# Optimization experiments

Hardware: AMD Instinct MI355X
Metric: run time of the kernel (lower is better)

## Reference

```python
import jax, jax.numpy as jnp
import numpy as np

B_, N, C, H = 8192, 49, 192, 6
HD = C // H
SCALE = HD ** -0.5


def setup_inputs() -> dict:
    key = jax.random.key(0)
    k0, k1, k2, k3 = jax.random.split(key, 4)
    x = jax.random.normal(k0, (B_, N, C), dtype=jnp.float32)
    mask = jax.random.randint(k1, (B_, N), 0, 2, dtype=jnp.int32)
    w_qkv = jax.random.normal(k2, (C, 3 * C), dtype=jnp.float32) * 0.02
    b_qkv = jnp.zeros((3 * C,), dtype=jnp.float32)
    w_proj = jax.random.normal(k3, (C, C), dtype=jnp.float32) * 0.02
    b_proj = jnp.zeros((C,), dtype=jnp.float32)
    return {"x": x, "mask": mask, "w_qkv": w_qkv, "b_qkv": b_qkv,
            "w_proj": w_proj, "b_proj": b_proj}


def reference(x, mask, w_qkv, b_qkv, w_proj, b_proj):
    # qkv projection: [B_, N, 3C] -> [3, B_, H, N, HD]
    qkv = (x @ w_qkv + b_qkv).reshape(B_, N, 3, H, HD).transpose(2, 0, 3, 1, 4)
    q, k, v = qkv[0], qkv[1], qkv[2]
    # scaled QK^T: [B_, H, N, N]
    attn = jnp.einsum('bhnd,bhmd->bhnm', q, k) * SCALE
    # additive key mask: mask==0 positions get -inf
    attn = jnp.where(mask[:, None, None, :] == 0, -jnp.inf, attn)
    p = jax.nn.softmax(attn, axis=-1)  # dropout p=0 -> identity
    out = jnp.einsum('bhnm,bhmd->bhnd', p, v)  # AV
    out = out.transpose(0, 2, 1, 3).reshape(B_, N, C)
    return out @ w_proj + b_proj
```

## Files before the change

kernel.cpp:

```cpp
#include <hip/hip_runtime.h>


typedef __attribute__((ext_vector_type(8))) short short8;
typedef __attribute__((ext_vector_type(4))) float f32x4;

#define SCALE 0.17677669529663687f

__device__ __forceinline__ unsigned short f2bf(float x) {
    union { float f; unsigned int i; } v; v.f = x;
    return (unsigned short)((v.i + 0x7FFFu + ((v.i >> 16) & 1u)) >> 16);
}

__device__ __forceinline__ unsigned int pkbf(float lo, float hi) {
    unsigned int r;
    asm("v_cvt_pk_bf16_f32 %0, %1, %2" : "=v"(r) : "v"(lo), "v"(hi));
    return r;
}

__device__ __forceinline__ int swz64(int row, int col) {
    return row * 64 + ((((col >> 3) ^ (row & 7)) << 3) | (col & 7));
}

__device__ __forceinline__ short8 xpose(f32x4 tlo, f32x4 thi, int srcA, bool hi) {
    unsigned int pl0 = pkbf(tlo[0], tlo[1]);
    unsigned int pl1 = pkbf(tlo[2], tlo[3]);
    unsigned int ph0 = pkbf(thi[0], thi[1]);
    unsigned int ph1 = pkbf(thi[2], thi[3]);
    unsigned int a0 = (unsigned int)__shfl((int)pl0, srcA);
    unsigned int b0 = (unsigned int)__shfl((int)ph0, srcA);
    unsigned int a1 = (unsigned int)__shfl((int)pl1, srcA);
    unsigned int b1 = (unsigned int)__shfl((int)ph1, srcA);
    unsigned int a2 = (unsigned int)__shfl((int)pl0, srcA + 16);
    unsigned int b2 = (unsigned int)__shfl((int)ph0, srcA + 16);
    unsigned int a3 = (unsigned int)__shfl((int)pl1, srcA + 16);
    unsigned int b3 = (unsigned int)__shfl((int)ph1, srcA + 16);
    union { short8 s8; unsigned int u[4]; } f;
    f.u[0] = hi ? b0 : a0;
    f.u[1] = hi ? b1 : a1;
    f.u[2] = hi ? b2 : a2;
    f.u[3] = hi ? b3 : a3;
    return f.s8;
}

__global__ void repack_kernel(const float* __restrict__ wqkv,
                              const float* __restrict__ wproj,
                              unsigned short* __restrict__ wq_pack,
                              unsigned short* __restrict__ wp_pack) {
    int idx = blockIdx.x * 256 + threadIdx.x;
    if (idx < 6 * 576 * 32) {
        int kk  = idx & 31;
        int col = (idx >> 5) % 576;
        int kt  = idx / (576 * 32);
        wq_pack[idx] = f2bf(wqkv[(kt * 32 + kk) * 576 + col]);
    } else {
        int j = idx - 6 * 576 * 32;
        if (j < 6 * 192 * 32) {
            int kk  = j & 31;
            int col = (j >> 5) % 192;
            int kt  = j / (192 * 32);
            wp_pack[j] = f2bf(wproj[(kt * 32 + kk) * 192 + col]);
        }
    }
}

__global__ __launch_bounds__(384)
void win_attn_kernel(const float* __restrict__ x,
                     const int* __restrict__ mask,
                     const float* __restrict__ bqkv,
                     const float* __restrict__ bproj,
                     const unsigned short* __restrict__ wq,
                     const unsigned short* __restrict__ wpj,
                     float* __restrict__ out) {
    __shared__ __align__(16) unsigned short region[25088];
    __shared__ __align__(16) float mbias[64];

    const int b    = blockIdx.x;
    const int tid  = threadIdx.x;
    const int lane = tid & 63;
    const int h    = tid >> 6;
    const int quad = lane >> 4;
    const int l16  = lane & 15;

    const float* xb = x + (size_t)b * 9408;
    for (int i4 = tid; i4 < 2352; i4 += 384) {
        int flat = i4 * 4;
        int n = flat / 192, c = flat % 192;
        float4 v = *(const float4*)(const void*)&xb[flat];
        uint2 pk;
        pk.x = pkbf(v.x, v.y);
        pk.y = pkbf(v.z, v.w);
        *(uint2*)(void*)&region[n * 200 + c] = pk;
    }
    if (tid < 375) {
        uint4 z = {0u, 0u, 0u, 0u};
        *(uint4*)(void*)&region[9800 + tid * 8] = z;
    }
    if (tid < 64)
        mbias[tid] = (tid < 49 && mask[b * 49 + tid] != 0) ? 0.0f : -1e30f;
    __syncthreads();

    f32x4 acc[6][4];
    #pragma unroll
    for (int t = 0; t < 6; ++t)
        #pragma unroll
        for (int mt = 0; mt < 4; ++mt)
            acc[t][mt] = (f32x4){0.f, 0.f, 0.f, 0.f};

    int colb[6];
    #pragma unroll
    for (int t = 0; t < 6; ++t) colb[t] = (t >> 1) * 192 + h * 32 + (t & 1) * 16;

    #pragma unroll
    for (int kt = 0; kt < 6; ++kt) {
        short8 af[4];
        #pragma unroll
        for (int mt = 0; mt < 4; ++mt)
            af[mt] = *(const short8*)(const void*)
                     &region[(mt * 16 + l16) * 200 + kt * 32 + quad * 8];
        #pragma unroll
        for (int t = 0; t < 6; ++t) {
            short8 bw = *(const short8*)(const void*)
                        &wq[(size_t)(kt * 576 + colb[t] + l16) * 32 + quad * 8];
            #pragma unroll
            for (int mt = 0; mt < 4; ++mt) {
                if (t < 4)
                    acc[t][mt] = __builtin_amdgcn_mfma_f32_16x16x32_bf16(
                                     bw, af[mt], acc[t][mt], 0, 0, 0);
                else
                    acc[t][mt] = __builtin_amdgcn_mfma_f32_16x16x32_bf16(
                                     af[mt], bw, acc[t][mt], 0, 0, 0);
            }
        }
    }
    #pragma unroll
    for (int t = 0; t < 4; ++t) {
        f32x4 bq = *(const f32x4*)(const void*)&bqkv[colb[t] + quad * 4];
        #pragma unroll
        for (int nt = 0; nt < 4; ++nt)
            #pragma unroll
            for (int r = 0; r < 4; ++r)
                acc[t][nt][r] += bq[r];
    }
    #pragma unroll
    for (int t = 4; t < 6; ++t) {
        float bv = bqkv[colb[t] + l16];
        #pragma unroll
        for (int mt = 0; mt < 4; ++mt)
            #pragma unroll
            for (int r = 0; r < 4; ++r)
                acc[t][mt][r] += bv;
    }

    unsigned short* vtb = &region[12800 + h * 2048];
    #pragma unroll
    for (int t = 0; t < 2; ++t)
        #pragma unroll
        for (int mt = 0; mt < 4; ++mt) {
            int d = t * 16 + l16;
            uint2 pk;
            pk.x = pkbf(acc[4 + t][mt][0], acc[4 + t][mt][1]);
            pk.y = pkbf(acc[4 + t][mt][2], acc[4 + t][mt][3]);
            *(uint2*)(void*)&vtb[swz64(d, mt * 16 + quad * 4)] = pk;
        }

    const int  srcA = ((lane & 16) << 1) | l16;
    const bool hiq  = (lane & 32) != 0;

    short8 qf[4], kf[4];
    #pragma unroll
    for (int nt = 0; nt < 4; ++nt) {
        qf[nt] = xpose(acc[0][nt], acc[1][nt], srcA, hiq);
        kf[nt] = xpose(acc[2][nt], acc[3][nt], srcA, hiq);
    }

    f32x4 s[4][4];
    #pragma unroll
    for (int mt = 0; mt < 4; ++mt)
        #pragma unroll
        for (int nt = 0; nt < 4; ++nt)
            s[mt][nt] = (f32x4){0.f, 0.f, 0.f, 0.f};
    #pragma unroll
    for (int mt = 0; mt < 4; ++mt)
        #pragma unroll
        for (int nt = 0; nt < 4; ++nt)
            s[mt][nt] = __builtin_amdgcn_mfma_f32_16x16x32_bf16(
                            kf[mt], qf[nt], s[mt][nt], 0, 0, 0);

    f32x4 mb4[4];
    #pragma unroll
    for (int mt = 0; mt < 4; ++mt)
        mb4[mt] = *(const f32x4*)(const void*)&mbias[mt * 16 + quad * 4];

    #pragma unroll
    for (int nt = 0; nt < 4; ++nt) {
        float ev[4][4];
        float pm[4];
        #pragma unroll
        for (int mt = 0; mt < 4; ++mt) {
            #pragma unroll
            for (int r = 0; r < 4; ++r)
                ev[mt][r] = s[mt][nt][r] * SCALE + mb4[mt][r];
            pm[mt] = fmaxf(fmaxf(ev[mt][0], ev[mt][1]),
                           fmaxf(ev[mt][2], ev[mt][3]));
        }
        float mx = fmaxf(fmaxf(pm[0], pm[1]), fmaxf(pm[2], pm[3]));
        mx = fmaxf(mx, __shfl_xor(mx, 16));
        mx = fmaxf(mx, __shfl_xor(mx, 32));
        float ps[4];
        #pragma unroll
        for (int mt = 0; mt < 4; ++mt) {
            #pragma unroll
            for (int r = 0; r < 4; ++r)
                ev[mt][r] = __expf(ev[mt][r] - mx);
            ps[mt] = (ev[mt][0] + ev[mt][1]) + (ev[mt][2] + ev[mt][3]);
        }
        float sum = (ps[0] + ps[1]) + (ps[2] + ps[3]);
        sum += __shfl_xor(sum, 16);
        sum += __shfl_xor(sum, 32);
        float inv = 1.0f / sum;
        #pragma unroll
        for (int mt = 0; mt < 4; ++mt)
            #pragma unroll
            for (int r = 0; r < 4; ++r)
                s[mt][nt][r] = ev[mt][r] * inv;
    }

    short8 ap[4][2];
    #pragma unroll
    for (int mo = 0; mo < 4; ++mo)
        #pragma unroll
        for (int kt = 0; kt < 2; ++kt)
            ap[mo][kt] = xpose(s[kt * 2][mo], s[kt * 2 + 1][mo], srcA, hiq);

    f32x4 o[4][2];
    #pragma unroll
    for (int mo = 0; mo < 4; ++mo)
        #pragma unroll
        for (int dt = 0; dt < 2; ++dt)
            o[mo][dt] = (f32x4){0.f, 0.f, 0.f, 0.f};

    #pragma unroll
    for (int kt = 0; kt < 2; ++kt) {
        short8 bvv[2];
        #pragma unroll
        for (int dt = 0; dt < 2; ++dt)
            bvv[dt] = *(const short8*)(const void*)
                      &vtb[swz64(dt * 16 + l16, kt * 32 + quad * 8)];
        #pragma unroll
        for (int mo = 0; mo < 4; ++mo)
            #pragma unroll
            for (int dt = 0; dt < 2; ++dt)
                o[mo][dt] = __builtin_amdgcn_mfma_f32_16x16x32_bf16(
                                ap[mo][kt], bvv[dt], o[mo][dt], 0, 0, 0);
    }

    __syncthreads();
    #pragma unroll
    for (int dt = 0; dt < 2; ++dt)
        #pragma unroll
        for (int mt = 0; mt < 4; ++mt)
            #pragma unroll
            for (int r = 0; r < 4; ++r)
                region[(mt * 16 + quad * 4 + r) * 200 + h * 32 + dt * 16 + l16]
                    = f2bf(o[mt][dt][r]);
    __syncthreads();

    f32x4 po[2][4];
    #pragma unroll
    for (int nt = 0; nt < 2; ++nt)
        #pragma unroll
        for (int mt = 0; mt < 4; ++mt)
            po[nt][mt] = (f32x4){0.f, 0.f, 0.f, 0.f};

    #pragma unroll
    for (int kt = 0; kt < 6; ++kt) {
        short8 ao[4];
        #pragma unroll
        for (int mt = 0; mt < 4; ++mt)
            ao[mt] = *(const short8*)(const void*)
                     &region[(mt * 16 + l16) * 200 + kt * 32 + quad * 8];
        #pragma unroll
        for (int nt = 0; nt < 2; ++nt) {
            int col = h * 32 + nt * 16 + l16;
            short8 bw = *(const short8*)(const void*)
                        &wpj[(size_t)(kt * 192 + col) * 32 + quad * 8];
            #pragma unroll
            for (int mt = 0; mt < 4; ++mt)
                po[nt][mt] = __builtin_amdgcn_mfma_f32_16x16x32_bf16(
                                 ao[mt], bw, po[nt][mt], 0, 0, 0);
        }
    }

    #pragma unroll
    for (int nt = 0; nt < 2; ++nt) {
        int col = h * 32 + nt * 16 + l16;
        float bv = bproj[col];
        #pragma unroll
        for (int mt = 0; mt < 4; ++mt)
            #pragma unroll
            for (int r = 0; r < 4; ++r) {
                int row = mt * 16 + quad * 4 + r;
                if (row < 49)
                    out[(size_t)b * 9408 + row * 192 + col] = po[nt][mt][r] + bv;
            }
    }
}

extern "C" void kernel_launch(void* const* d_in, const int* in_sizes, int n_in,
                              void* d_out, int out_size, void* d_ws, size_t ws_size,
                              hipStream_t stream) {
    const float* x      = (const float*)d_in[0];
    const int*   mask   = (const int*)d_in[1];
    const float* w_qkv  = (const float*)d_in[2];
    const float* b_qkv  = (const float*)d_in[3];
    const float* w_proj = (const float*)d_in[4];
    const float* b_proj = (const float*)d_in[5];
    float*       out    = (float*)d_out;

    unsigned short* wq_pack = (unsigned short*)d_ws;
    unsigned short* wp_pack = wq_pack + 110592;

    repack_kernel<<<(110592 + 36864 + 255) / 256, 256, 0, stream>>>(
        w_qkv, w_proj, wq_pack, wp_pack);
    win_attn_kernel<<<8192, 384, 0, stream>>>(x, mask, b_qkv, b_proj,
                                              wq_pack, wp_pack, out);
}
```

Before: 850.4 us.

## Split QKV GEMM into QK and V phases and stream scores per column tile

The fused QKV projection accumulator (24 f32x4 tiles) is split into a Q/K phase and a separate V phase, and the V results are packed to LDS straight after their own GEMM. The QK^T scores are now computed one column tile at a time inside the softmax loop and transposed into bf16 fragments immediately, so the full 16-tile score array is never live. The goal is lower peak VGPR pressure and higher occupancy. The cost is that the x fragments are reloaded from LDS for the second GEMM pass, and the MFMA chains become shorter, giving less interleaving.

```diff
diff --git a/kernel.cpp b/kernel.cpp
--- a/kernel.cpp
+++ b/kernel.cpp
@@ -99,109 +99,118 @@
         mbias[tid] = (tid < 49 && mask[b * 49 + tid] != 0) ? 0.0f : -1e30f;
     __syncthreads();
 
-    f32x4 acc[6][4];
-    #pragma unroll
-    for (int t = 0; t < 6; ++t)
-        #pragma unroll
-        for (int mt = 0; mt < 4; ++mt)
-            acc[t][mt] = (f32x4){0.f, 0.f, 0.f, 0.f};
+    const int  srcA = ((lane & 16) << 1) | l16;
+    const bool hiq  = (lane & 32) != 0;
 
     int colb[6];
     #pragma unroll
     for (int t = 0; t < 6; ++t) colb[t] = (t >> 1) * 192 + h * 32 + (t & 1) * 16;
 
-    #pragma unroll
-    for (int kt = 0; kt < 6; ++kt) {
-        short8 af[4];
-        #pragma unroll
-        for (int mt = 0; mt < 4; ++mt)
-            af[mt] = *(const short8*)(const void*)
-                     &region[(mt * 16 + l16) * 200 + kt * 32 + quad * 8];
-        #pragma unroll
-        for (int t = 0; t < 6; ++t) {
-            short8 bw = *(const short8*)(const void*)
-                        &wq[(size_t)(kt * 576 + colb[t] + l16) * 32 + quad * 8];
-            #pragma unroll
-            for (int mt = 0; mt < 4; ++mt) {
-                if (t < 4)
+    short8 qf[4], kf[4];
+    {
+        f32x4 acc[4][4];
+        #pragma unroll
+        for (int t = 0; t < 4; ++t)
+            #pragma unroll
+            for (int mt = 0; mt < 4; ++mt)
+                acc[t][mt] = (f32x4){0.f, 0.f, 0.f, 0.f};
+
+        #pragma unroll
+        for (int kt = 0; kt < 6; ++kt) {
+            short8 af[4];
+            #pragma unroll
+            for (int mt = 0; mt < 4; ++mt)
+                af[mt] = *(const short8*)(const void*)
+                         &region[(mt * 16 + l16) * 200 + kt * 32 + quad * 8];
+            #pragma unroll
+            for (int t = 0; t < 4; ++t) {
+                short8 bw = *(const short8*)(const void*)
+                            &wq[(size_t)(kt * 576 + colb[t] + l16) * 32 + quad * 8];
+                #pragma unroll
+                for (int mt = 0; mt < 4; ++mt)
                     acc[t][mt] = __builtin_amdgcn_mfma_f32_16x16x32_bf16(
                                      bw, af[mt], acc[t][mt], 0, 0, 0);
-                else
-                    acc[t][mt] = __builtin_amdgcn_mfma_f32_16x16x32_bf16(
-                                     af[mt], bw, acc[t][mt], 0, 0, 0);
             }
         }
-    }
-    #pragma unroll
-    for (int t = 0; t < 4; ++t) {
-        f32x4 bq = *(const f32x4*)(const void*)&bqkv[colb[t] + quad * 4];
-        #pragma unroll
-        for (int nt = 0; nt < 4; ++nt)
-            #pragma unroll
-            for (int r = 0; r < 4; ++r)
-                acc[t][nt][r] += bq[r];
-    }
-    #pragma unroll
-    for (int t = 4; t < 6; ++t) {
-        float bv = bqkv[colb[t] + l16];
-        #pragma unroll
-        for (int mt = 0; mt < 4; ++mt)
-            #pragma unroll
-            for (int r = 0; r < 4; ++r)
-                acc[t][mt][r] += bv;
+        #pragma unroll
+        for (int t = 0; t < 4; ++t) {
+            f32x4 bq = *(const f32x4*)(const void*)&bqkv[colb[t] + quad * 4];
+            #pragma unroll
+            for (int nt = 0; nt < 4; ++nt)
+                #pragma unroll
+                for (int r = 0; r < 4; ++r)
+                    acc[t][nt][r] += bq[r];
+        }
+        #pragma unroll
+        for (int nt = 0; nt < 4; ++nt) {
+            qf[nt] = xpose(acc[0][nt], acc[1][nt], srcA, hiq);
+            kf[nt] = xpose(acc[2][nt], acc[3][nt], srcA, hiq);
+        }
     }
 
     unsigned short* vtb = &region[12800 + h * 2048];
-    #pragma unroll
-    for (int t = 0; t < 2; ++t)
-        #pragma unroll
-        for (int mt = 0; mt < 4; ++mt) {
-            int d = t * 16 + l16;
-            uint2 pk;
-            pk.x = pkbf(acc[4 + t][mt][0], acc[4 + t][mt][1]);
-            pk.y = pkbf(acc[4 + t][mt][2], acc[4 + t][mt][3]);
-            *(uint2*)(void*)&vtb[swz64(d, mt * 16 + quad * 4)] = pk;
-        }
-
-    const int  srcA = ((lane & 16) << 1) | l16;
-    const bool hiq  = (lane & 32) != 0;
-
-    short8 qf[4], kf[4];
-    #pragma unroll
-    for (int nt = 0; nt < 4; ++nt) {
-        qf[nt] = xpose(acc[0][nt], acc[1][nt], srcA, hiq);
-        kf[nt] = xpose(acc[2][nt], acc[3][nt], srcA, hiq);
-    }
-
-    f32x4 s[4][4];
-    #pragma unroll
-    for (int mt = 0; mt < 4; ++mt)
-        #pragma unroll
-        for (int nt = 0; nt < 4; ++nt)
-            s[mt][nt] = (f32x4){0.f, 0.f, 0.f, 0.f};
-    #pragma unroll
-    for (int mt = 0; mt < 4; ++mt)
-        #pragma unroll
-        for (int nt = 0; nt < 4; ++nt)
-            s[mt][nt] = __builtin_amdgcn_mfma_f32_16x16x32_bf16(
-                            kf[mt], qf[nt], s[mt][nt], 0, 0, 0);
+    {
+        f32x4 accv[2][4];
+        #pragma unroll
+        for (int t = 0; t < 2; ++t)
+            #pragma unroll
+            for (int mt = 0; mt < 4; ++mt)
+                accv[t][mt] = (f32x4){0.f, 0.f, 0.f, 0.f};
+
+        #pragma unroll
+        for (int kt = 0; kt < 6; ++kt) {
+            short8 af[4];
+            #pragma unroll
+            for (int mt = 0; mt < 4; ++mt)
+                af[mt] = *(const short8*)(const void*)
+                         &region[(mt * 16 + l16) * 200 + kt * 32 + quad * 8];
+            #pragma unroll
+            for (int t = 0; t < 2; ++t) {
+                short8 bw = *(const short8*)(const void*)
+                            &wq[(size_t)(kt * 576 + colb[4 + t] + l16) * 32 + quad * 8];
+                #pragma unroll
+                for (int mt = 0; mt < 4; ++mt)
+                    accv[t][mt] = __builtin_amdgcn_mfma_f32_16x16x32_bf16(
+                                      af[mt], bw, accv[t][mt], 0, 0, 0);
+            }
+        }
+        #pragma unroll
+        for (int t = 0; t < 2; ++t) {
+            float bv = bqkv[colb[4 + t] + l16];
+            #pragma unroll
+            for (int mt = 0; mt < 4; ++mt) {
+                int d = t * 16 + l16;
+                uint2 pk;
+                pk.x = pkbf(accv[t][mt][0] + bv, accv[t][mt][1] + bv);
+                pk.y = pkbf(accv[t][mt][2] + bv, accv[t][mt][3] + bv);
+                *(uint2*)(void*)&vtb[swz64(d, mt * 16 + quad * 4)] = pk;
+            }
+        }
+    }
 
     f32x4 mb4[4];
     #pragma unroll
     for (int mt = 0; mt < 4; ++mt)
         mb4[mt] = *(const f32x4*)(const void*)&mbias[mt * 16 + quad * 4];
 
+    short8 ap[4][2];
     #pragma unroll
     for (int nt = 0; nt < 4; ++nt) {
-        float ev[4][4];
+        f32x4 sr[4];
+        #pragma unroll
+        for (int mt = 0; mt < 4; ++mt) {
+            sr[mt] = (f32x4){0.f, 0.f, 0.f, 0.f};
+            sr[mt] = __builtin_amdgcn_mfma_f32_16x16x32_bf16(
+                         kf[mt], qf[nt], sr[mt], 0, 0, 0);
+        }
         float pm[4];
         #pragma unroll
         for (int mt = 0; mt < 4; ++mt) {
             #pragma unroll
             for (int r = 0; r < 4; ++r)
-                ev[mt][r] = s[mt][nt][r] * SCALE + mb4[mt][r];
-            pm[mt] = fmaxf(fmaxf(ev[mt][0], ev[mt][1]),
-                           fmaxf(ev[mt][2], ev[mt][3]));
+                sr[mt][r] = sr[mt][r] * SCALE + mb4[mt][r];
+            pm[mt] = fmaxf(fmaxf(sr[mt][0], sr[mt][1]),
+                           fmaxf(sr[mt][2], sr[mt][3]));
         }
         float mx = fmaxf(fmaxf(pm[0], pm[1]), fmaxf(pm[2], pm[3]));
         mx = fmaxf(mx, __shfl_xor(mx, 16));
@@ -211,8 +220,8 @@
         for (int mt = 0; mt < 4; ++mt) {
             #pragma unroll
             for (int r = 0; r < 4; ++r)
-                ev[mt][r] = __expf(ev[mt][r] - mx);
-            ps[mt] = (ev[mt][0] + ev[mt][1]) + (ev[mt][2] + ev[mt][3]);
+                sr[mt][r] = __expf(sr[mt][r] - mx);
+            ps[mt] = (sr[mt][0] + sr[mt][1]) + (sr[mt][2] + sr[mt][3]);
         }
         float sum = (ps[0] + ps[1]) + (ps[2] + ps[3]);
         sum += __shfl_xor(sum, 16);
@@ -222,15 +231,10 @@
         for (int mt = 0; mt < 4; ++mt)
             #pragma unroll
             for (int r = 0; r < 4; ++r)
-                s[mt][nt][r] = ev[mt][r] * inv;
-    }
-
-    short8 ap[4][2];
-    #pragma unroll
-    for (int mo = 0; mo < 4; ++mo)
-        #pragma unroll
-        for (int kt = 0; kt < 2; ++kt)
-            ap[mo][kt] = xpose(s[kt * 2][mo], s[kt * 2 + 1][mo], srcA, hiq);
+                sr[mt][r] *= inv;
+        ap[nt][0] = xpose(sr[0], sr[1], srcA, hiq);
+        ap[nt][1] = xpose(sr[2], sr[3], srcA, hiq);
+    }
 
     f32x4 o[4][2];
     #pragma unroll
```

Result: no change. 848.7 us (-0.2%).
